# Kernel tuning notes

Hardware: AMD Instinct MI355X
Metric: run time of the kernel (lower is better)

The kernel has to match this reference:

```python
import jax, jax.numpy as jnp
import numpy as np
from jax import lax

NUM_VARS = 16384
NUM_CHECKS = 8192
BATCH = 32
MAX_ITER = 15
H_DENSITY = 0.001  # ~8 ones per column, LDPC-like Tanner graph


def setup_inputs() -> dict:
    key = jax.random.key(0)
    k_h, k_s, k_l = jax.random.split(key, 3)
    # Sparse binary parity-check matrix represented densely (same math).
    parity_matrix = (jax.random.uniform(k_h, (NUM_CHECKS, NUM_VARS)) < H_DENSITY).astype(jnp.float32)
    syndrome = jax.random.randint(k_s, (BATCH, NUM_CHECKS), 0, 2).astype(jnp.float32)
    channel_llrs = jax.random.normal(k_l, (BATCH, NUM_VARS), dtype=jnp.float32)
    w_vc = jnp.ones((1,), dtype=jnp.float32)
    w_cv = jnp.ones((1,), dtype=jnp.float32)
    damping = jnp.float32(0.5)
    return {
        "syndrome": syndrome,
        "parity_matrix": parity_matrix,
        "channel_llrs": channel_llrs,
        "w_vc": w_vc,
        "w_cv": w_cv,
        "damping": damping,
    }


def reference(syndrome, parity_matrix, channel_llrs, w_vc, w_cv, damping):
    # syndrome: (B, C); parity_matrix H: (C, V); channel_llrs: (B, V)
    s_sign = 1.0 - 2.0 * syndrome  # (B, C)

    def body(v_beliefs, _):
        # v -> c: sparse.mm(H, v^T)^T == v @ H^T  -> (B, C)
        v_to_c = w_vc * (v_beliefs @ parity_matrix.T)
        c_msg = s_sign * jnp.tanh(v_to_c * 0.5)  # (B, C)
        # c -> v: sparse.mm(H^T, c^T)^T == c @ H  -> (B, V)
        c_to_v = w_cv * (c_msg @ parity_matrix)
        v_new = damping * v_beliefs + (1.0 - damping) * (channel_llrs + c_to_v)
        return v_new, None

    v_beliefs, _ = lax.scan(body, channel_llrs, None, length=MAX_ITER)
    return jax.nn.sigmoid(-v_beliefs)  # (B, V) bit-flip probabilities
```

## Files before the change

### kernel.cpp

```cpp
#include <hip/hip_runtime.h>


#define C_NUM 8192
#define V_NUM 16384
#define B_NUM 32
#define RW 64
#define CW 32

#define RQ 12
#define CQ 8
#define RQ_S 13
#define CQ_S 9

#define NBLK 256
#define NTHR 1024

#define NBLK_A 2048
#define NTHR_A 256
#define NT_A (NBLK_A * NTHR_A)

#define WCAP 256

#define BEL_SL (16400 * 4)
#define CMS_SL (8200 * 4)

typedef unsigned short u16;
typedef unsigned int u32;
typedef unsigned long long u64;

#define NBAR 32
#define BAR_STRIDE 64

__device__ __forceinline__ float agent_ldf(const float* p) {
    return __hip_atomic_load(p, __ATOMIC_RELAXED, __HIP_MEMORY_SCOPE_AGENT);
}
__device__ __forceinline__ void agent_stf(float* p, float v) {
    __hip_atomic_store(p, v, __ATOMIC_RELAXED, __HIP_MEMORY_SCOPE_AGENT);
}
__device__ __forceinline__ u64 agent_ld64(const u64* p) {
    return __hip_atomic_load(p, __ATOMIC_RELAXED, __HIP_MEMORY_SCOPE_AGENT);
}
__device__ __forceinline__ int agent_ldi(const int* p) {
    return __hip_atomic_load(p, __ATOMIC_RELAXED, __HIP_MEMORY_SCOPE_AGENT);
}
__device__ __forceinline__ void agent_st16(u16* p, u16 v) {
    __hip_atomic_store(p, v, __ATOMIC_RELAXED, __HIP_MEMORY_SCOPE_AGENT);
}

__device__ __forceinline__ void grid_barrier(u32* bars, int id) {
    __syncthreads();
    if (threadIdx.x == 0) {
        u32* base = bars + id * 8 * BAR_STRIDE;
        asm volatile("s_waitcnt vmcnt(0) lgkmcnt(0)" ::: "memory");
        __hip_atomic_fetch_add(base + (blockIdx.x & 7) * BAR_STRIDE, 1u,
                               __ATOMIC_RELAXED, __HIP_MEMORY_SCOPE_AGENT);
        u32 sum;
        do {
            sum = 0;
#pragma unroll
            for (int g = 0; g < 8; ++g)
                sum += __hip_atomic_load(base + g * BAR_STRIDE,
                                         __ATOMIC_RELAXED, __HIP_MEMORY_SCOPE_AGENT);
            if (sum < (u32)NBLK) __builtin_amdgcn_s_sleep(4);
        } while (sum < (u32)NBLK);
        asm volatile("" ::: "memory");
    }
    __syncthreads();
}

__device__ __forceinline__ float fast_tanh_half(float x) {
    float ax = fabsf(x);
    float e = __expf(-ax);
    return copysignf((1.0f - e) / (1.0f + e), x);
}

template<bool LOCAL>
__device__ __forceinline__ float sum16(const float* __restrict__ base,
                                       const u64* __restrict__ q4, int b4) {
    const float* a[16];
#pragma unroll
    for (int p = 0; p < 4; ++p) {
        u64 q = q4[p];
        a[4 * p + 0] = base + (int)(q & 0xFFFFu) * 4 + b4;
        a[4 * p + 1] = base + (int)((q >> 16) & 0xFFFFu) * 4 + b4;
        a[4 * p + 2] = base + (int)((q >> 32) & 0xFFFFu) * 4 + b4;
        a[4 * p + 3] = base + (int)(q >> 48) * 4 + b4;
    }
    float r[16];
    if (LOCAL) {
        asm volatile(
            "global_load_dword %0, %16, off sc0\n\t"
            "global_load_dword %1, %17, off sc0\n\t"
            "global_load_dword %2, %18, off sc0\n\t"
            "global_load_dword %3, %19, off sc0\n\t"
            "global_load_dword %4, %20, off sc0\n\t"
            "global_load_dword %5, %21, off sc0\n\t"
            "global_load_dword %6, %22, off sc0\n\t"
            "global_load_dword %7, %23, off sc0\n\t"
            "global_load_dword %8, %24, off sc0\n\t"
            "global_load_dword %9, %25, off sc0\n\t"
            "global_load_dword %10, %26, off sc0\n\t"
            "global_load_dword %11, %27, off sc0\n\t"
            "global_load_dword %12, %28, off sc0\n\t"
            "global_load_dword %13, %29, off sc0\n\t"
            "global_load_dword %14, %30, off sc0\n\t"
            "global_load_dword %15, %31, off sc0\n\t"
            "s_waitcnt vmcnt(0)"
            : "=&v"(r[0]), "=&v"(r[1]), "=&v"(r[2]), "=&v"(r[3]),
              "=&v"(r[4]), "=&v"(r[5]), "=&v"(r[6]), "=&v"(r[7]),
              "=&v"(r[8]), "=&v"(r[9]), "=&v"(r[10]), "=&v"(r[11]),
              "=&v"(r[12]), "=&v"(r[13]), "=&v"(r[14]), "=&v"(r[15])
            : "v"(a[0]), "v"(a[1]), "v"(a[2]), "v"(a[3]),
              "v"(a[4]), "v"(a[5]), "v"(a[6]), "v"(a[7]),
              "v"(a[8]), "v"(a[9]), "v"(a[10]), "v"(a[11]),
              "v"(a[12]), "v"(a[13]), "v"(a[14]), "v"(a[15])
            : "memory");
    } else {
#pragma unroll
        for (int j = 0; j < 16; ++j) r[j] = agent_ldf(a[j]);
    }
    float s0 = (r[0] + r[1]) + (r[2] + r[3]);
    float s1 = (r[4] + r[5]) + (r[6] + r[7]);
    float s2 = (r[8] + r[9]) + (r[10] + r[11]);
    float s3 = (r[12] + r[13]) + (r[14] + r[15]);
    return (s0 + s1) + (s2 + s3);
}

__global__ __launch_bounds__(NTHR_A, 8)
void scan_build(const float* __restrict__ H,
                int* __restrict__ row_cnt, int* __restrict__ col_cnt,
                u16* __restrict__ row_idx, u16* __restrict__ col_idx) {
    __shared__ u32 lds_edges[(NTHR_A / 64) * WCAP];
    const int lane = threadIdx.x & 63;
    u32* const wl = lds_edges + (threadIdx.x >> 6) * WCAP;
    const u64 ltmask = (1ull << lane) - 1ull;
    const float4* Hv = (const float4*)H;
    const u32 t0 = blockIdx.x * NTHR_A + threadIdx.x;
    int wb = 0;
#pragma unroll 1
    for (int i = 0; i < 8; ++i) {
        float4 h[8];
#pragma unroll
        for (int k = 0; k < 8; ++k)
            h[k] = Hv[t0 + (u32)(i * 8 + k) * (u32)NT_A];
#pragma unroll
        for (int k = 0; k < 8; ++k) {
            u32 eb = (t0 + (u32)(i * 8 + k) * (u32)NT_A) * 4u;
            float vals[4] = {h[k].x, h[k].y, h[k].z, h[k].w};
#pragma unroll
            for (int kk = 0; kk < 4; ++kk) {
                bool nz = vals[kk] != 0.0f;
                u64 bb = __ballot(nz);
                if (bb) {
                    if (nz) {
                        int off = wb + (int)__popcll(bb & ltmask);
                        if (off < WCAP) wl[off] = eb + kk;
                    }
                    wb += (int)__popcll(bb);
                }
            }
        }
    }
    int wave_cnt = wb < WCAP ? wb : WCAP;
    for (int e = lane; e < wave_cnt; e += 64) {
        u32 ee = wl[e];
        int c = (int)(ee >> 14);
        int v = (int)(ee & (V_NUM - 1));
        int rs = atomicAdd(&row_cnt[c], 1);
        if (rs < RW) agent_st16(&row_idx[(size_t)c * RW + rs], (u16)v);
        int cs = atomicAdd(&col_cnt[v], 1);
        if (cs < CW) agent_st16(&col_idx[(size_t)v * CW + cs], (u16)c);
    }
}

template<bool LOCAL>
__device__ __forceinline__ void decode_tail(
    int G, int R,
    const float* __restrict__ synd, const float* __restrict__ llr,
    const int* __restrict__ row_cnt, const int* __restrict__ col_cnt,
    const u16* __restrict__ row_idx, const u16* __restrict__ col_idx,
    float* __restrict__ bel_x, float* __restrict__ cms_x,
    u32* __restrict__ bars, float* __restrict__ out,
    u64* ls_row, u64* ls_col,
    float wvc, float wcv, float d)
{
    const int t = threadIdx.x;
    const int b4 = t & 3;
    const int qid = t >> 2;
    float* const belS = bel_x + (size_t)G * BEL_SL;
    float* const cmsS = cms_x + (size_t)G * CMS_SL;

    for (int e = t; e < 256 * RQ; e += NTHR) {
        int rl = e / RQ, p = e - rl * RQ;
        int c = (R << 8) + rl;
        int n = agent_ldi(&row_cnt[c]); n = n > 4 * RQ ? 4 * RQ : n;
        u64 q = agent_ld64(&((const u64*)(row_idx + (size_t)c * RW))[p]);
        int j = 4 * p;
        u64 a0 = (j + 0 < n) ? (q & 0xFFFFu) : (u64)V_NUM;
        u64 a1 = (j + 1 < n) ? ((q >> 16) & 0xFFFFu) : (u64)V_NUM;
        u64 a2 = (j + 2 < n) ? ((q >> 32) & 0xFFFFu) : (u64)V_NUM;
        u64 a3 = (j + 3 < n) ? (q >> 48) : (u64)V_NUM;
        ls_row[rl * RQ_S + p] = a0 | (a1 << 16) | (a2 << 32) | (a3 << 48);
    }
    for (int e = t; e < 512 * CQ; e += NTHR) {
        int gl = e >> 3, p = e & 7;
        int v = (gl < 256) ? ((R << 8) + gl) : (C_NUM + (R << 8) + (gl - 256));
        int n = agent_ldi(&col_cnt[v]); n = n > 4 * CQ ? 4 * CQ : n;
        u64 q = agent_ld64(&((const u64*)(col_idx + (size_t)v * CW))[p]);
        int j = 4 * p;
        u64 a0 = (j + 0 < n) ? (q & 0xFFFFu) : (u64)C_NUM;
        u64 a1 = (j + 1 < n) ? ((q >> 16) & 0xFFFFu) : (u64)C_NUM;
        u64 a2 = (j + 2 < n) ? ((q >> 32) & 0xFFFFu) : (u64)C_NUM;
        u64 a3 = (j + 3 < n) ? (q >> 48) : (u64)C_NUM;
        ls_col[gl * CQ_S + p] = a0 | (a1 << 16) | (a2 << 32) | (a3 << 48);
    }
    const int c_my = (R << 8) + qid;
    const int v0_my = (R << 8) + qid;
    const int v1_my = C_NUM + (R << 8) + qid;
    int nrow;  { int n = agent_ldi(&row_cnt[c_my]);  nrow  = n > 4*RQ ? 4*RQ : n; }
    int ncol0; { int n = agent_ldi(&col_cnt[v0_my]); ncol0 = n > 4*CQ ? 4*CQ : n; }
    int ncol1; { int n = agent_ldi(&col_cnt[v1_my]); ncol1 = n > 4*CQ ? 4*CQ : n; }
    const int b = (G << 2) + b4;
    const float ss = 1.0f - 2.0f * synd[b * C_NUM + c_my];
    const float llr0 = llr[b * V_NUM + v0_my];
    const float llr1 = llr[b * V_NUM + v1_my];
    float bel0 = llr0, bel1 = llr1;
    if (LOCAL) {
        belS[v0_my * 4 + b4] = bel0;
        belS[v1_my * 4 + b4] = bel1;
    } else {
        agent_stf(&belS[v0_my * 4 + b4], bel0);
        agent_stf(&belS[v1_my * 4 + b4], bel1);
    }

    grid_barrier(bars, 1);

    const u64* const rowL  = ls_row + qid * RQ_S;
    const u64* const colL0 = ls_col + qid * CQ_S;
    const u64* const colL1 = ls_col + (256 + qid) * CQ_S;
    float* const cms_own  = cmsS + c_my * 4 + b4;
    float* const bel_own0 = belS + v0_my * 4 + b4;
    float* const bel_own1 = belS + v1_my * 4 + b4;

    int barid = 2;
    for (int it = 0; it < 15; ++it) {
        {
            float sum = sum16<LOCAL>(belS, rowL, b4);
            if (__any(nrow > 16)) sum += sum16<LOCAL>(belS, rowL + 4, b4);
            if (__any(nrow > 32)) sum += sum16<LOCAL>(belS, rowL + 8, b4);
            float m = ss * fast_tanh_half(wvc * sum);
            if (LOCAL) *cms_own = m; else agent_stf(cms_own, m);
        }
        grid_barrier(bars, barid++);

        bool last = (it == 14);
        float sum0 = sum16<LOCAL>(cmsS, colL0, b4);
        if (__any(ncol0 > 16)) sum0 += sum16<LOCAL>(cmsS, colL0 + 4, b4);
        float sum1 = sum16<LOCAL>(cmsS, colL1, b4);
        if (__any(ncol1 > 16)) sum1 += sum16<LOCAL>(cmsS, colL1 + 4, b4);

        float nb0 = d * bel0 + (1.0f - d) * (llr0 + wcv * sum0);
        float nb1 = d * bel1 + (1.0f - d) * (llr1 + wcv * sum1);
        bel0 = nb0; bel1 = nb1;
        if (!last) {
            if (LOCAL) { *bel_own0 = nb0; *bel_own1 = nb1; }
            else { agent_stf(bel_own0, nb0); agent_stf(bel_own1, nb1); }
            grid_barrier(bars, barid++);
        } else {
            out[b * V_NUM + v0_my] = 1.0f / (1.0f + __expf(nb0));
            out[b * V_NUM + v1_my] = 1.0f / (1.0f + __expf(nb1));
        }
    }
}

__global__ __launch_bounds__(NTHR, 1) __attribute__((amdgpu_waves_per_eu(4, 4)))
void bp_decode(const float* __restrict__ synd,
               const float* __restrict__ llr,
               const float* __restrict__ w_vc_p,
               const float* __restrict__ w_cv_p,
               const float* __restrict__ damp_p,
               const int* __restrict__ row_cnt, const int* __restrict__ col_cnt,
               const u16* __restrict__ row_idx, const u16* __restrict__ col_idx,
               float* __restrict__ bel_x, float* __restrict__ cms_x,
               u32* __restrict__ bars, int* __restrict__ xcd_cnt,
               float* __restrict__ out) {
    const int t = threadIdx.x;
    const int tid = blockIdx.x * NTHR + t;

    __shared__ u64 shpool[10496];
    __shared__ int s_xcd, s_rank;
    u64* const ls_row = shpool;
    u64* const ls_col = shpool + 256 * RQ_S;

    if (t == 0) {
        u32 x;
        asm volatile("s_getreg_b32 %0, hwreg(HW_REG_XCC_ID)" : "=s"(x));
        x &= 15;
        s_xcd = (int)x;
        s_rank = atomicAdd(&xcd_cnt[x], 1);
    }
    if (tid < 32) {
        int g = tid >> 2, j = tid & 3;
        agent_stf(&bel_x[(size_t)g * BEL_SL + V_NUM * 4 + j], 0.0f);
    } else if (tid < 64) {
        int g = (tid - 32) >> 2, j = tid & 3;
        agent_stf(&cms_x[(size_t)g * CMS_SL + C_NUM * 4 + j], 0.0f);
    }
    grid_barrier(bars, 0);

    bool balanced = true;
#pragma unroll
    for (int g = 0; g < 8; ++g) balanced &= (agent_ldi(&xcd_cnt[g]) == 32);

    const float wvc = w_vc_p[0];
    const float wcv = w_cv_p[0];
    const float d   = damp_p[0];

    if (balanced) {
        decode_tail<true>(s_xcd, s_rank, synd, llr, row_cnt, col_cnt,
                          row_idx, col_idx, bel_x, cms_x, bars, out,
                          ls_row, ls_col, wvc, wcv, d);
    } else {
        decode_tail<false>((int)(blockIdx.x >> 5), (int)(blockIdx.x & 31),
                           synd, llr, row_cnt, col_cnt,
                           row_idx, col_idx, bel_x, cms_x, bars, out,
                           ls_row, ls_col, wvc, wcv, d);
    }
}

extern "C" void kernel_launch(void* const* d_in, const int* in_sizes, int n_in,
                              void* d_out, int out_size, void* d_ws, size_t ws_size,
                              hipStream_t stream) {
    const float* synd = (const float*)d_in[0];
    const float* H    = (const float*)d_in[1];
    const float* llr  = (const float*)d_in[2];
    const float* w_vc = (const float*)d_in[3];
    const float* w_cv = (const float*)d_in[4];
    const float* damp = (const float*)d_in[5];
    float* out = (float*)d_out;

    char* ws = (char*)d_ws;
    size_t off = 0;
    int* row_cnt = (int*)(ws + off); off += (size_t)C_NUM * 4;
    int* col_cnt = (int*)(ws + off); off += (size_t)V_NUM * 4;
    u16* row_idx = (u16*)(ws + off); off += (size_t)C_NUM * RW * 2;
    u16* col_idx = (u16*)(ws + off); off += (size_t)V_NUM * CW * 2;
    float* bel_x = (float*)(ws + off); off += (size_t)8 * BEL_SL * 4;
    float* cms_x = (float*)(ws + off); off += (size_t)8 * CMS_SL * 4;
    u32* bars  = (u32*)(ws + off); off += (size_t)NBAR * 8 * BAR_STRIDE * 4;
    int* xcd_cnt = (int*)(ws + off); off += 64;

    hipMemsetAsync(row_cnt, 0, (size_t)(C_NUM + V_NUM) * 4, stream);
    hipMemsetAsync(bars, 0, (size_t)NBAR * 8 * BAR_STRIDE * 4 + 64, stream);

    hipLaunchKernelGGL(scan_build, dim3(NBLK_A), dim3(NTHR_A), 0, stream,
                       H, row_cnt, col_cnt, row_idx, col_idx);

    void* args[] = {
        (void*)&synd, (void*)&llr, (void*)&w_vc, (void*)&w_cv, (void*)&damp,
        (void*)&row_cnt, (void*)&col_cnt, (void*)&row_idx, (void*)&col_idx,
        (void*)&bel_x, (void*)&cms_x, (void*)&bars, (void*)&xcd_cnt,
        (void*)&out
    };
    hipLaunchCooperativeKernel((const void*)bp_decode,
                               dim3(NBLK), dim3(NTHR), args, 0, stream);
}
```

Before: 947.8 us.

## Fuse sparse-index build into cooperative decode kernel and use per-XCD barriers

Moves the dense H scan that builds the row and column adjacency lists into the cooperative decode kernel, removing a separate kernel launch. The scan prefetches H in software-pipelined pairs of float4 loads. In the balanced case the per-iteration grid-wide barriers are replaced with barriers local to one XCD, since each XCD handles its own batch slice. The cost is that all of H must be streamed by only 256 blocks, with less occupancy than the separate 2048-block scan had, and the amdgpu_waves_per_eu attribute is dropped.

```diff
diff --git a/kernel.cpp b/kernel.cpp
--- a/kernel.cpp
+++ b/kernel.cpp
@@ -14,10 +14,7 @@
 
 #define NBLK 256
 #define NTHR 1024
-
-#define NBLK_A 2048
-#define NTHR_A 256
-#define NT_A (NBLK_A * NTHR_A)
+#define NTH (NBLK * NTHR)
 
 #define WCAP 256
 
@@ -30,6 +27,8 @@
 
 #define NBAR 32
 #define BAR_STRIDE 64
+#define NIDS 32
+#define XB_STRIDE 16
 
 __device__ __forceinline__ float agent_ldf(const float* p) {
     return __hip_atomic_load(p, __ATOMIC_RELAXED, __HIP_MEMORY_SCOPE_AGENT);
@@ -63,6 +62,20 @@
                                          __ATOMIC_RELAXED, __HIP_MEMORY_SCOPE_AGENT);
             if (sum < (u32)NBLK) __builtin_amdgcn_s_sleep(4);
         } while (sum < (u32)NBLK);
+        asm volatile("" ::: "memory");
+    }
+    __syncthreads();
+}
+
+__device__ __forceinline__ void xcd_barrier(u32* cnt) {
+    __syncthreads();
+    if (threadIdx.x == 0) {
+        asm volatile("s_waitcnt vmcnt(0) lgkmcnt(0)" ::: "memory");
+        __hip_atomic_fetch_add(cnt, 1u, __ATOMIC_RELAXED,
+                               __HIP_MEMORY_SCOPE_AGENT);
+        while (__hip_atomic_load(cnt, __ATOMIC_RELAXED,
+                                 __HIP_MEMORY_SCOPE_AGENT) < 32u)
+            __builtin_amdgcn_s_sleep(2);
         asm volatile("" ::: "memory");
     }
     __syncthreads();
@@ -126,53 +139,6 @@
     return (s0 + s1) + (s2 + s3);
 }
 
-__global__ __launch_bounds__(NTHR_A, 8)
-void scan_build(const float* __restrict__ H,
-                int* __restrict__ row_cnt, int* __restrict__ col_cnt,
-                u16* __restrict__ row_idx, u16* __restrict__ col_idx) {
-    __shared__ u32 lds_edges[(NTHR_A / 64) * WCAP];
-    const int lane = threadIdx.x & 63;
-    u32* const wl = lds_edges + (threadIdx.x >> 6) * WCAP;
-    const u64 ltmask = (1ull << lane) - 1ull;
-    const float4* Hv = (const float4*)H;
-    const u32 t0 = blockIdx.x * NTHR_A + threadIdx.x;
-    int wb = 0;
-#pragma unroll 1
-    for (int i = 0; i < 8; ++i) {
-        float4 h[8];
-#pragma unroll
-        for (int k = 0; k < 8; ++k)
-            h[k] = Hv[t0 + (u32)(i * 8 + k) * (u32)NT_A];
-#pragma unroll
-        for (int k = 0; k < 8; ++k) {
-            u32 eb = (t0 + (u32)(i * 8 + k) * (u32)NT_A) * 4u;
-            float vals[4] = {h[k].x, h[k].y, h[k].z, h[k].w};
-#pragma unroll
-            for (int kk = 0; kk < 4; ++kk) {
-                bool nz = vals[kk] != 0.0f;
-                u64 bb = __ballot(nz);
-                if (bb) {
-                    if (nz) {
-                        int off = wb + (int)__popcll(bb & ltmask);
-                        if (off < WCAP) wl[off] = eb + kk;
-                    }
-                    wb += (int)__popcll(bb);
-                }
-            }
-        }
-    }
-    int wave_cnt = wb < WCAP ? wb : WCAP;
-    for (int e = lane; e < wave_cnt; e += 64) {
-        u32 ee = wl[e];
-        int c = (int)(ee >> 14);
-        int v = (int)(ee & (V_NUM - 1));
-        int rs = atomicAdd(&row_cnt[c], 1);
-        if (rs < RW) agent_st16(&row_idx[(size_t)c * RW + rs], (u16)v);
-        int cs = atomicAdd(&col_cnt[v], 1);
-        if (cs < CW) agent_st16(&col_idx[(size_t)v * CW + cs], (u16)c);
-    }
-}
-
 template<bool LOCAL>
 __device__ __forceinline__ void decode_tail(
     int G, int R,
@@ -180,7 +146,8 @@
     const int* __restrict__ row_cnt, const int* __restrict__ col_cnt,
     const u16* __restrict__ row_idx, const u16* __restrict__ col_idx,
     float* __restrict__ bel_x, float* __restrict__ cms_x,
-    u32* __restrict__ bars, float* __restrict__ out,
+    u32* __restrict__ bars, u32* __restrict__ xb,
+    float* __restrict__ out,
     u64* ls_row, u64* ls_col,
     float wvc, float wcv, float d)
 {
@@ -233,7 +200,7 @@
         agent_stf(&belS[v1_my * 4 + b4], bel1);
     }
 
-    grid_barrier(bars, 1);
+    if (LOCAL) xcd_barrier(xb); else grid_barrier(bars, 2);
 
     const u64* const rowL  = ls_row + qid * RQ_S;
     const u64* const colL0 = ls_col + qid * CQ_S;
@@ -242,7 +209,7 @@
     float* const bel_own0 = belS + v0_my * 4 + b4;
     float* const bel_own1 = belS + v1_my * 4 + b4;
 
-    int barid = 2;
+    int barid = 1;
     for (int it = 0; it < 15; ++it) {
         {
             float sum = sum16<LOCAL>(belS, rowL, b4);
@@ -251,7 +218,9 @@
             float m = ss * fast_tanh_half(wvc * sum);
             if (LOCAL) *cms_own = m; else agent_stf(cms_own, m);
         }
-        grid_barrier(bars, barid++);
+        if (LOCAL) xcd_barrier(xb + barid * XB_STRIDE);
+        else grid_barrier(bars, 2 + barid);
+        ++barid;
 
         bool last = (it == 14);
         float sum0 = sum16<LOCAL>(cmsS, colL0, b4);
@@ -265,7 +234,9 @@
         if (!last) {
             if (LOCAL) { *bel_own0 = nb0; *bel_own1 = nb1; }
             else { agent_stf(bel_own0, nb0); agent_stf(bel_own1, nb1); }
-            grid_barrier(bars, barid++);
+            if (LOCAL) xcd_barrier(xb + barid * XB_STRIDE);
+            else grid_barrier(bars, 2 + barid);
+            ++barid;
         } else {
             out[b * V_NUM + v0_my] = 1.0f / (1.0f + __expf(nb0));
             out[b * V_NUM + v1_my] = 1.0f / (1.0f + __expf(nb1));
@@ -273,24 +244,28 @@
     }
 }
 
-__global__ __launch_bounds__(NTHR, 1) __attribute__((amdgpu_waves_per_eu(4, 4)))
-void bp_decode(const float* __restrict__ synd,
-               const float* __restrict__ llr,
-               const float* __restrict__ w_vc_p,
-               const float* __restrict__ w_cv_p,
-               const float* __restrict__ damp_p,
-               const int* __restrict__ row_cnt, const int* __restrict__ col_cnt,
-               const u16* __restrict__ row_idx, const u16* __restrict__ col_idx,
-               float* __restrict__ bel_x, float* __restrict__ cms_x,
-               u32* __restrict__ bars, int* __restrict__ xcd_cnt,
-               float* __restrict__ out) {
+__global__ __launch_bounds__(NTHR, 1)
+void bp_fused(const float* __restrict__ H,
+              const float* __restrict__ synd,
+              const float* __restrict__ llr,
+              const float* __restrict__ w_vc_p,
+              const float* __restrict__ w_cv_p,
+              const float* __restrict__ damp_p,
+              int* __restrict__ row_cnt, int* __restrict__ col_cnt,
+              u16* __restrict__ row_idx, u16* __restrict__ col_idx,
+              float* __restrict__ bel_x, float* __restrict__ cms_x,
+              u32* __restrict__ bars, u32* __restrict__ xbars,
+              int* __restrict__ xcd_cnt,
+              float* __restrict__ out) {
     const int t = threadIdx.x;
     const int tid = blockIdx.x * NTHR + t;
-
-    __shared__ u64 shpool[10496];
+    const int lane = t & 63;
+
+    __shared__ u32 lds_edges[(NTHR / 64) * WCAP + 1024];
+    __shared__ u64 ls_row[256 * RQ_S];
+    __shared__ u64 ls_col[512 * CQ_S];
     __shared__ int s_xcd, s_rank;
-    u64* const ls_row = shpool;
-    u64* const ls_col = shpool + 256 * RQ_S;
+    u32* const wl = lds_edges + (t >> 6) * WCAP;
 
     if (t == 0) {
         u32 x;
@@ -306,8 +281,56 @@
         int g = (tid - 32) >> 2, j = tid & 3;
         agent_stf(&cms_x[(size_t)g * CMS_SL + C_NUM * 4 + j], 0.0f);
     }
+
+    int wave_cnt;
+    {
+        const float4* Hv = (const float4*)H;
+        const u64 ltmask = (1ull << lane) - 1ull;
+        int wb = 0;
+        int ta = tid;
+        int tb = tid + 2 * NTH;
+        float4 a0 = Hv[ta], a1 = Hv[ta + NTH];
+        float4 b0 = Hv[tb], b1 = Hv[tb + NTH];
+#pragma unroll 1
+        for (int itn = 0; itn < 64; ++itn) {
+            int tc = tb + 2 * NTH;
+            float4 p0, p1;
+            if (itn < 62) { p0 = Hv[tc]; p1 = Hv[tc + NTH]; }
+            float vals[8] = {a0.x, a0.y, a0.z, a0.w, a1.x, a1.y, a1.z, a1.w};
+#pragma unroll
+            for (int k = 0; k < 8; ++k) {
+                bool nz = vals[k] != 0.0f;
+                u64 bb = __ballot(nz);
+                if (bb) {
+                    if (nz) {
+                        int ee = (k < 4) ? (ta * 4 + k)
+                                         : ((ta + NTH) * 4 + (k - 4));
+                        int off = wb + (int)__popcll(bb & ltmask);
+                        if (off < WCAP) wl[off] = (u32)ee;
+                    }
+                    wb += (int)__popcll(bb);
+                }
+            }
+            a0 = b0; a1 = b1; b0 = p0; b1 = p1; ta = tb; tb = tc;
+        }
+        wave_cnt = wb < WCAP ? wb : WCAP;
+    }
     grid_barrier(bars, 0);
 
+    {
+        for (int e = lane; e < wave_cnt; e += 64) {
+            u32 ee = wl[e];
+            int c = (int)(ee >> 14);
+            int v = (int)(ee & (V_NUM - 1));
+            int rs = atomicAdd(&row_cnt[c], 1);
+            if (rs < RW) agent_st16(&row_idx[(size_t)c * RW + rs], (u16)v);
+            int cs = atomicAdd(&col_cnt[v], 1);
+            if (cs < CW) agent_st16(&col_idx[(size_t)v * CW + cs], (u16)c);
+        }
+    }
+    grid_barrier(bars, 1);
+
+    int my_xcd = s_xcd, my_rank = s_rank;
     bool balanced = true;
 #pragma unroll
     for (int g = 0; g < 8; ++g) balanced &= (agent_ldi(&xcd_cnt[g]) == 32);
@@ -317,13 +340,14 @@
     const float d   = damp_p[0];
 
     if (balanced) {
-        decode_tail<true>(s_xcd, s_rank, synd, llr, row_cnt, col_cnt,
-                          row_idx, col_idx, bel_x, cms_x, bars, out,
+        u32* xb = xbars + (size_t)my_xcd * NIDS * XB_STRIDE;
+        decode_tail<true>(my_xcd, my_rank, synd, llr, row_cnt, col_cnt,
+                          row_idx, col_idx, bel_x, cms_x, bars, xb, out,
                           ls_row, ls_col, wvc, wcv, d);
     } else {
         decode_tail<false>((int)(blockIdx.x >> 5), (int)(blockIdx.x & 31),
                            synd, llr, row_cnt, col_cnt,
-                           row_idx, col_idx, bel_x, cms_x, bars, out,
+                           row_idx, col_idx, bel_x, cms_x, bars, nullptr, out,
                            ls_row, ls_col, wvc, wcv, d);
     }
 }
@@ -348,20 +372,21 @@
     float* bel_x = (float*)(ws + off); off += (size_t)8 * BEL_SL * 4;
     float* cms_x = (float*)(ws + off); off += (size_t)8 * CMS_SL * 4;
     u32* bars  = (u32*)(ws + off); off += (size_t)NBAR * 8 * BAR_STRIDE * 4;
+    u32* xbars = (u32*)(ws + off); off += (size_t)8 * NIDS * XB_STRIDE * 4;
     int* xcd_cnt = (int*)(ws + off); off += 64;
 
     hipMemsetAsync(row_cnt, 0, (size_t)(C_NUM + V_NUM) * 4, stream);
-    hipMemsetAsync(bars, 0, (size_t)NBAR * 8 * BAR_STRIDE * 4 + 64, stream);
-
-    hipLaunchKernelGGL(scan_build, dim3(NBLK_A), dim3(NTHR_A), 0, stream,
-                       H, row_cnt, col_cnt, row_idx, col_idx);
+    hipMemsetAsync(bars, 0,
+                   (size_t)NBAR * 8 * BAR_STRIDE * 4
+                 + (size_t)8 * NIDS * XB_STRIDE * 4 + 64, stream);
 
     void* args[] = {
-        (void*)&synd, (void*)&llr, (void*)&w_vc, (void*)&w_cv, (void*)&damp,
+        (void*)&H, (void*)&synd, (void*)&llr,
+        (void*)&w_vc, (void*)&w_cv, (void*)&damp,
         (void*)&row_cnt, (void*)&col_cnt, (void*)&row_idx, (void*)&col_idx,
-        (void*)&bel_x, (void*)&cms_x, (void*)&bars, (void*)&xcd_cnt,
-        (void*)&out
+        (void*)&bel_x, (void*)&cms_x, (void*)&bars, (void*)&xbars,
+        (void*)&xcd_cnt, (void*)&out
     };
-    hipLaunchCooperativeKernel((const void*)bp_decode,
+    hipLaunchCooperativeKernel((const void*)bp_fused,
                                dim3(NBLK), dim3(NTHR), args, 0, stream);
 }
```

Result: faster. 890.1 us (-6.1%).
